# Performance work log

Measured on AMD Instinct MI355X. Metric: run time of the kernel, lower is better.

## Reference

```python
import jax, jax.numpy as jnp
import numpy as np

TAU = 1.0

def setup_inputs() -> dict:
    key = jax.random.key(0)
    k1, k2 = jax.random.split(key)
    b, t, n, e, top_k = 2, 64, 1024, 512, 256
    x = jax.random.normal(k1, (b, t, n, e), dtype=jnp.float32)
    # torch nn.Linear(embed_size, top_k): weight [top_k, e], bias [top_k]
    W = jax.random.normal(k2, (top_k, e), dtype=jnp.float32) * (1.0 / np.sqrt(e))
    b_bias = jnp.zeros((top_k,), dtype=jnp.float32)
    return {"x": x, "W": W, "b_bias": b_bias}

def reference(x, W, b_bias):
    b, t, n, e = x.shape
    x_flat = x.reshape(b, t * n, e)                 # [b, m, e], m = t*n
    scores = x_flat @ W.T + b_bias                  # [b, m, top_k]
    weights = jax.nn.softmax(scores / TAU, axis=1)  # softmax over token axis m
    # weighted-sum pooling for all top_k slots at once (replaces torch loop)
    selected = jnp.einsum('bmk,bme->bke', weights, x_flat)  # [b, top_k, e]
    return selected
```

## Files before the change

kernel.cpp:

```cpp
#include <hip/hip_runtime.h>
#include <stdint.h>

#define B_DIM 2
#define M_DIM 65536
#define E_DIM 512
#define K_DIM 256

typedef __bf16 bf16_t;
typedef __bf16 bf16x8 __attribute__((ext_vector_type(8)));
typedef float  f32x4  __attribute__((ext_vector_type(4)));

typedef const __attribute__((address_space(1))) void* gas_ptr;
typedef __attribute__((address_space(3))) void* las_ptr;

__device__ __forceinline__ void async_load16(const void* g, void* l) {
    __builtin_amdgcn_global_load_lds((gas_ptr)g, (las_ptr)l, 16, 0, 0);
}

__device__ __forceinline__ unsigned short bf16_bits(float f) {
    return __builtin_bit_cast(unsigned short, (__bf16)f);
}
__device__ __forceinline__ unsigned int pack2(float lo, float hi) {
    return (unsigned int)bf16_bits(lo) | ((unsigned int)bf16_bits(hi) << 16);
}

__global__ __launch_bounds__(256) void cast_w(const float* __restrict__ W, bf16_t* __restrict__ Wb) {
    int idx = blockIdx.x * 256 + threadIdx.x;
    float4 v = ((const float4*)W)[idx];
    ((uint2*)Wb)[idx] = make_uint2(pack2(v.x, v.y), pack2(v.z, v.w));
}

__global__ __launch_bounds__(256) void gemm1_exp_t(const float* __restrict__ x, const bf16_t* __restrict__ Wb,
                                                   bf16_t* __restrict__ pb, float* __restrict__ psums,
                                                   bf16_t* __restrict__ xT) {
    int gid = blockIdx.x;
    int mt = gid & 1023;
    int b  = gid >> 10;
    int m0 = mt * 64;
    int t = threadIdx.x, lane = t & 63, w = t >> 6;

    __shared__ __align__(16) char smem[40960];
    bf16_t* Alds = (bf16_t*)smem;
    bf16_t* Blds = (bf16_t*)(smem + 32768);
    bf16_t* Elds = (bf16_t*)smem;

    const float* xb = x + ((size_t)b * M_DIM + m0) * E_DIM;

    f32x4 zero = {0.f, 0.f, 0.f, 0.f};
    f32x4 acc[4][4];
#pragma unroll
    for (int i = 0; i < 4; ++i)
#pragma unroll
        for (int j = 0; j < 4; ++j) acc[i][j] = zero;

    int bst_r = t >> 2, bst_s0 = t & 3;

    int q = lane >> 4, r15 = lane & 15;

    for (int ke = 0; ke < 8; ++ke) {
        int e0 = ke * 64;
#pragma unroll
        for (int is = 0; is < 8; ++is) {
            int c = is * 256 + t;
            int row = c >> 3, sl = c & 7;
            int ge = sl ^ (row & 7);
            async_load16(Wb + (size_t)row * E_DIM + e0 + ge * 8, Alds + c * 8);
        }
#pragma unroll
        for (int sg = 0; sg < 2; ++sg) {
            int sl = bst_s0 + sg * 4;
            int ge = sl ^ (bst_r & 7);
            const float4* f = (const float4*)(xb + (size_t)bst_r * E_DIM + e0 + ge * 8);
            float4 a0 = f[0], a1 = f[1];
            *(uint4*)(Blds + bst_r * 64 + sl * 8) =
                make_uint4(pack2(a0.x, a0.y), pack2(a0.z, a0.w), pack2(a1.x, a1.y), pack2(a1.z, a1.w));
        }
        __syncthreads();

#pragma unroll
        for (int h = 0; h < 2; ++h) {
            bf16x8 af[4], bfr[4];
#pragma unroll
            for (int i = 0; i < 4; ++i) {
                int r = w * 64 + i * 16 + r15;
                int sl = (h * 4 + q) ^ (r & 7);
                af[i] = *(const bf16x8*)(Alds + r * 64 + sl * 8);
            }
#pragma unroll
            for (int j = 0; j < 4; ++j) {
                int r = j * 16 + r15;
                int sl = (h * 4 + q) ^ (r & 7);
                bfr[j] = *(const bf16x8*)(Blds + r * 64 + sl * 8);
            }
#pragma unroll
            for (int i = 0; i < 4; ++i)
#pragma unroll
                for (int j = 0; j < 4; ++j)
                    acc[i][j] = __builtin_amdgcn_mfma_f32_16x16x32_bf16(af[i], bfr[j], acc[i][j], 0, 0, 0);
        }

        {
            const unsigned short* Bs = (const unsigned short*)Blds;
            int l7 = t & 7;
            int mbase = l7 * 8;
            int ebase = t >> 3;
#pragma unroll
            for (int p = 0; p < 2; ++p) {
                int ecol = p * 32 + ebase;
                unsigned short vs[8];
#pragma unroll
                for (int s = 0; s < 8; ++s) {
                    int mmr = (s + l7) & 7;
                    int sl = (ecol >> 3) ^ mmr;
                    vs[mmr] = Bs[(mbase + mmr) * 64 + sl * 8 + (ecol & 7)];
                }
                uint4 u = make_uint4((unsigned)vs[0] | ((unsigned)vs[1] << 16),
                                     (unsigned)vs[2] | ((unsigned)vs[3] << 16),
                                     (unsigned)vs[4] | ((unsigned)vs[5] << 16),
                                     (unsigned)vs[6] | ((unsigned)vs[7] << 16));
                *(uint4*)(xT + ((size_t)(b * E_DIM + e0 + ecol)) * M_DIM + m0 + mbase) = u;
            }
        }
        __syncthreads();
    }

    int cc = lane & 15;
    float ksum[4][4];
#pragma unroll
    for (int i = 0; i < 4; ++i)
#pragma unroll
        for (int p = 0; p < 4; ++p) ksum[i][p] = 0.f;

#pragma unroll
    for (int i = 0; i < 4; ++i) {
        int kr = w * 64 + i * 16 + q * 4;
#pragma unroll
        for (int j = 0; j < 4; ++j) {
            int colb = j * 16 + cc;
            int g = colb >> 3, off = colb & 7;
#pragma unroll
            for (int p = 0; p < 4; ++p) {
                float v = __expf(acc[i][j][p]);
                ksum[i][p] += v;
                int k = kr + p;
                Elds[k * 64 + ((g ^ (k & 7)) * 8) + off] = (bf16_t)v;
            }
        }
    }
#pragma unroll
    for (int mask = 1; mask < 16; mask <<= 1)
#pragma unroll
        for (int i = 0; i < 4; ++i)
#pragma unroll
            for (int p = 0; p < 4; ++p)
                ksum[i][p] += __shfl_xor(ksum[i][p], mask, 64);
    if (cc == 0) {
        float* pp = psums + ((size_t)b * 1024 + mt) * 256;
#pragma unroll
        for (int i = 0; i < 4; ++i)
#pragma unroll
            for (int p = 0; p < 4; ++p)
                pp[w * 64 + i * 16 + q * 4 + p] = ksum[i][p];
    }
    __syncthreads();

    {
        int g = t & 7, rsub = t >> 3;
        uint4* dstb = (uint4*)(pb + (size_t)b * K_DIM * M_DIM + m0);
#pragma unroll
        for (int p = 0; p < 8; ++p) {
            int k = p * 32 + rsub;
            uint4 u = *(const uint4*)(Elds + k * 64 + ((g ^ (k & 7)) * 8));
            dstb[((size_t)k * M_DIM + g * 8) >> 3] = u;
        }
    }
}

__global__ __launch_bounds__(256) void gemm2(const bf16_t* __restrict__ pb, const bf16_t* __restrict__ xT,
                                             float* __restrict__ part) {
    int bid = blockIdx.x;
    int kt = bid & 1, et = (bid >> 1) & 3, ch = (bid >> 3) & 31, b = bid >> 8;
    int t = threadIdx.x, lane = t & 63, w = t >> 6;
    int wk = w & 1, we = w >> 1;

    __shared__ __align__(16) bf16_t Alds[128 * 64];
    __shared__ __align__(16) bf16_t Blds[128 * 64];

    const bf16_t* Ab = pb + ((size_t)(b * K_DIM + kt * 128)) * M_DIM + ch * 2048;
    const bf16_t* Bb = xT + ((size_t)(b * E_DIM + et * 128)) * M_DIM + ch * 2048;

    f32x4 zero = {0.f, 0.f, 0.f, 0.f};
    f32x4 acc[4][4];
#pragma unroll
    for (int i = 0; i < 4; ++i)
#pragma unroll
        for (int j = 0; j < 4; ++j) acc[i][j] = zero;

    int q = lane >> 4, r15 = lane & 15;

    for (int km = 0; km < 32; ++km) {
        int m0 = km * 64;
#pragma unroll
        for (int is = 0; is < 4; ++is) {
            int c = is * 256 + t;
            int row = c >> 3, sl = c & 7;
            int ge = sl ^ (row & 7);
            async_load16(Ab + (size_t)row * M_DIM + m0 + ge * 8, Alds + c * 8);
            async_load16(Bb + (size_t)row * M_DIM + m0 + ge * 8, Blds + c * 8);
        }
        __syncthreads();

#pragma unroll
        for (int h = 0; h < 2; ++h) {
            bf16x8 af[4], bfr[4];
#pragma unroll
            for (int i = 0; i < 4; ++i) {
                int r = wk * 64 + i * 16 + r15;
                int sl = (h * 4 + q) ^ (r & 7);
                af[i] = *(const bf16x8*)(Alds + r * 64 + sl * 8);
            }
#pragma unroll
            for (int j = 0; j < 4; ++j) {
                int r = we * 64 + j * 16 + r15;
                int sl = (h * 4 + q) ^ (r & 7);
                bfr[j] = *(const bf16x8*)(Blds + r * 64 + sl * 8);
            }
#pragma unroll
            for (int i = 0; i < 4; ++i)
#pragma unroll
                for (int j = 0; j < 4; ++j)
                    acc[i][j] = __builtin_amdgcn_mfma_f32_16x16x32_bf16(af[i], bfr[j], acc[i][j], 0, 0, 0);
        }
        __syncthreads();
    }

    float* pp = part + (size_t)bid * 16384;
    int cc = lane & 15;
#pragma unroll
    for (int i = 0; i < 4; ++i)
#pragma unroll
        for (int p = 0; p < 4; ++p) {
            int kl = wk * 64 + i * 16 + q * 4 + p;
#pragma unroll
            for (int j = 0; j < 4; ++j) {
                int el = we * 64 + j * 16 + cc;
                pp[kl * 128 + el] = acc[i][j][p];
            }
        }
}

__global__ __launch_bounds__(256) void reduce_out(const float* __restrict__ part, const float* __restrict__ psums,
                                                  float* __restrict__ out) {
    int bid = blockIdx.x;
    int ehalf = bid & 1, k = (bid >> 1) & 255, b = bid >> 9;
    int t = threadIdx.x, lane = t & 63;

    float cs = 0.f;
#pragma unroll
    for (int c = 0; c < 4; ++c) {
        int mt = c * 256 + t;
        cs += psums[((size_t)b * 1024 + mt) * 256 + k];
    }
#pragma unroll
    for (int mask = 1; mask < 64; mask <<= 1) cs += __shfl_xor(cs, mask, 64);
    __shared__ float cspart[4];
    if (lane == 0) cspart[t >> 6] = cs;
    __syncthreads();
    float colsum = (cspart[0] + cspart[1]) + (cspart[2] + cspart[3]);

    int e = ehalf * 256 + t;
    int kt = k >> 7, kl = k & 127, et = e >> 7, el = e & 127;
    float s = 0.f;
#pragma unroll
    for (int ch = 0; ch < 32; ++ch) {
        int bid2 = kt | (et << 1) | (ch << 3) | (b << 8);
        s += part[(size_t)bid2 * 16384 + kl * 128 + el];
    }
    out[((size_t)(b * 256 + k)) * 512 + e] = s / colsum;
}

extern "C" void kernel_launch(void* const* d_in, const int* in_sizes, int n_in,
                              void* d_out, int out_size, void* d_ws, size_t ws_size,
                              hipStream_t stream) {
    (void)in_sizes; (void)n_in; (void)out_size; (void)ws_size;
    const float* x = (const float*)d_in[0];
    const float* W = (const float*)d_in[1];

    char* ws = (char*)d_ws;
    bf16_t* xT    = (bf16_t*)ws;
    bf16_t* Wb    = (bf16_t*)(ws + 134217728);
    bf16_t* pb    = (bf16_t*)(ws + 134479872);
    float*  psums = (float*)(ws + 201588736);
    float*  part  = (float*)(ws + 203685888);
    float*  out   = (float*)d_out;

    cast_w<<<128, 256, 0, stream>>>(W, Wb);
    gemm1_exp_t<<<2048, 256, 0, stream>>>(x, Wb, pb, psums, xT);
    gemm2<<<512, 256, 0, stream>>>(pb, xT, part);
    reduce_out<<<1024, 256, 0, stream>>>(part, psums, out);
}
```

Measured before the change: 486.9 us.

## Store exp-weights and transposed x as FP8 and run second GEMM with FP8 MFMA

The intermediate exp-score matrix and the transposed copy of x are written as FP8 (e4m3/bf8 via cvt_pk_fp8) instead of bf16. The second GEMM then reads half the bytes and uses the fp8 MFMA instruction, with a new LDS swizzle for 8-byte fragments. This halves intermediate global traffic and increases MFMA throughput, but it sharply lowers precision of both operands, so accuracy may fall outside tolerance.

```diff
diff --git a/kernel.cpp b/kernel.cpp
--- a/kernel.cpp
+++ b/kernel.cpp
@@ -23,6 +23,16 @@
 __device__ __forceinline__ unsigned int pack2(float lo, float hi) {
     return (unsigned int)bf16_bits(lo) | ((unsigned int)bf16_bits(hi) << 16);
 }
+__device__ __forceinline__ float bf16u_to_f32(unsigned short us) {
+    return __builtin_bit_cast(float, (unsigned)us << 16);
+}
+__device__ __forceinline__ uint2 pack8_fp8(const float* f) {
+    int lo = __builtin_amdgcn_cvt_pk_fp8_f32(f[0], f[1], 0, false);
+    lo = __builtin_amdgcn_cvt_pk_fp8_f32(f[2], f[3], lo, true);
+    int hi = __builtin_amdgcn_cvt_pk_fp8_f32(f[4], f[5], 0, false);
+    hi = __builtin_amdgcn_cvt_pk_fp8_f32(f[6], f[7], hi, true);
+    return make_uint2((unsigned)lo, (unsigned)hi);
+}
 
 __global__ __launch_bounds__(256) void cast_w(const float* __restrict__ W, bf16_t* __restrict__ Wb) {
     int idx = blockIdx.x * 256 + threadIdx.x;
@@ -31,8 +41,8 @@
 }
 
 __global__ __launch_bounds__(256) void gemm1_exp_t(const float* __restrict__ x, const bf16_t* __restrict__ Wb,
-                                                   bf16_t* __restrict__ pb, float* __restrict__ psums,
-                                                   bf16_t* __restrict__ xT) {
+                                                   unsigned char* __restrict__ pb8, float* __restrict__ psums,
+                                                   unsigned char* __restrict__ xT8) {
     int gid = blockIdx.x;
     int mt = gid & 1023;
     int b  = gid >> 10;
@@ -107,18 +117,14 @@
 #pragma unroll
             for (int p = 0; p < 2; ++p) {
                 int ecol = p * 32 + ebase;
-                unsigned short vs[8];
+                float f[8];
 #pragma unroll
                 for (int s = 0; s < 8; ++s) {
                     int mmr = (s + l7) & 7;
                     int sl = (ecol >> 3) ^ mmr;
-                    vs[mmr] = Bs[(mbase + mmr) * 64 + sl * 8 + (ecol & 7)];
+                    f[mmr] = bf16u_to_f32(Bs[(mbase + mmr) * 64 + sl * 8 + (ecol & 7)]);
                 }
-                uint4 u = make_uint4((unsigned)vs[0] | ((unsigned)vs[1] << 16),
-                                     (unsigned)vs[2] | ((unsigned)vs[3] << 16),
-                                     (unsigned)vs[4] | ((unsigned)vs[5] << 16),
-                                     (unsigned)vs[6] | ((unsigned)vs[7] << 16));
-                *(uint4*)(xT + ((size_t)(b * E_DIM + e0 + ecol)) * M_DIM + m0 + mbase) = u;
+                *(uint2*)(xT8 + ((size_t)(b * E_DIM + e0 + ecol)) * M_DIM + m0 + mbase) = pack8_fp8(f);
             }
         }
         __syncthreads();
@@ -166,28 +172,31 @@
 
     {
         int g = t & 7, rsub = t >> 3;
-        uint4* dstb = (uint4*)(pb + (size_t)b * K_DIM * M_DIM + m0);
+        unsigned char* dstb = pb8 + (size_t)b * K_DIM * M_DIM + m0;
 #pragma unroll
         for (int p = 0; p < 8; ++p) {
             int k = p * 32 + rsub;
-            uint4 u = *(const uint4*)(Elds + k * 64 + ((g ^ (k & 7)) * 8));
-            dstb[((size_t)k * M_DIM + g * 8) >> 3] = u;
-        }
-    }
-}
-
-__global__ __launch_bounds__(256) void gemm2(const bf16_t* __restrict__ pb, const bf16_t* __restrict__ xT,
+            const unsigned short* src = (const unsigned short*)(Elds + k * 64 + ((g ^ (k & 7)) * 8));
+            float f[8];
+#pragma unroll
+            for (int s = 0; s < 8; ++s) f[s] = bf16u_to_f32(src[s]);
+            *(uint2*)(dstb + (size_t)k * M_DIM + g * 8) = pack8_fp8(f);
+        }
+    }
+}
+
+__global__ __launch_bounds__(256) void gemm2(const unsigned char* __restrict__ pb8, const unsigned char* __restrict__ xT8,
                                              float* __restrict__ part) {
     int bid = blockIdx.x;
     int kt = bid & 1, et = (bid >> 1) & 3, ch = (bid >> 3) & 31, b = bid >> 8;
     int t = threadIdx.x, lane = t & 63, w = t >> 6;
     int wk = w & 1, we = w >> 1;
 
-    __shared__ __align__(16) bf16_t Alds[128 * 64];
-    __shared__ __align__(16) bf16_t Blds[128 * 64];
-
-    const bf16_t* Ab = pb + ((size_t)(b * K_DIM + kt * 128)) * M_DIM + ch * 2048;
-    const bf16_t* Bb = xT + ((size_t)(b * E_DIM + et * 128)) * M_DIM + ch * 2048;
+    __shared__ __align__(16) unsigned char Alds[128 * 64];
+    __shared__ __align__(16) unsigned char Blds[128 * 64];
+
+    const unsigned char* Ab = pb8 + ((size_t)(b * K_DIM + kt * 128)) * M_DIM + ch * 2048;
+    const unsigned char* Bb = xT8 + ((size_t)(b * E_DIM + et * 128)) * M_DIM + ch * 2048;
 
     f32x4 zero = {0.f, 0.f, 0.f, 0.f};
     f32x4 acc[4][4];
@@ -201,35 +210,40 @@
     for (int km = 0; km < 32; ++km) {
         int m0 = km * 64;
 #pragma unroll
-        for (int is = 0; is < 4; ++is) {
+        for (int is = 0; is < 2; ++is) {
             int c = is * 256 + t;
-            int row = c >> 3, sl = c & 7;
-            int ge = sl ^ (row & 7);
-            async_load16(Ab + (size_t)row * M_DIM + m0 + ge * 8, Alds + c * 8);
-            async_load16(Bb + (size_t)row * M_DIM + m0 + ge * 8, Blds + c * 8);
+            int row = c >> 2, a = c & 3;
+            int sr = (row & 3) ^ ((row >> 2) & 3);
+            int bsl = a ^ sr;
+            async_load16(Ab + (size_t)row * M_DIM + m0 + bsl * 16, Alds + c * 16);
+            async_load16(Bb + (size_t)row * M_DIM + m0 + bsl * 16, Blds + c * 16);
         }
         __syncthreads();
 
 #pragma unroll
         for (int h = 0; h < 2; ++h) {
-            bf16x8 af[4], bfr[4];
+            long av[4], bv[4];
 #pragma unroll
             for (int i = 0; i < 4; ++i) {
-                int r = wk * 64 + i * 16 + r15;
-                int sl = (h * 4 + q) ^ (r & 7);
-                af[i] = *(const bf16x8*)(Alds + r * 64 + sl * 8);
+                int r = wk * 128 / 2 * 0 + wk * 64 + i * 16 + r15;
+                int sr = (r & 3) ^ ((r >> 2) & 3);
+                int g = h * 4 + q;
+                int off = (((g >> 1) ^ sr) * 16) + (g & 1) * 8;
+                av[i] = *(const long*)(Alds + r * 64 + off);
             }
 #pragma unroll
             for (int j = 0; j < 4; ++j) {
                 int r = we * 64 + j * 16 + r15;
-                int sl = (h * 4 + q) ^ (r & 7);
-                bfr[j] = *(const bf16x8*)(Blds + r * 64 + sl * 8);
+                int sr = (r & 3) ^ ((r >> 2) & 3);
+                int g = h * 4 + q;
+                int off = (((g >> 1) ^ sr) * 16) + (g & 1) * 8;
+                bv[j] = *(const long*)(Blds + r * 64 + off);
             }
 #pragma unroll
             for (int i = 0; i < 4; ++i)
 #pragma unroll
                 for (int j = 0; j < 4; ++j)
-                    acc[i][j] = __builtin_amdgcn_mfma_f32_16x16x32_bf16(af[i], bfr[j], acc[i][j], 0, 0, 0);
+                    acc[i][j] = __builtin_amdgcn_mfma_f32_16x16x32_fp8_fp8(av[i], bv[j], acc[i][j], 0, 0, 0);
         }
         __syncthreads();
     }
@@ -287,15 +301,15 @@
     const float* W = (const float*)d_in[1];
 
     char* ws = (char*)d_ws;
-    bf16_t* xT    = (bf16_t*)ws;
-    bf16_t* Wb    = (bf16_t*)(ws + 134217728);
-    bf16_t* pb    = (bf16_t*)(ws + 134479872);
-    float*  psums = (float*)(ws + 201588736);
-    float*  part  = (float*)(ws + 203685888);
+    unsigned char* xT8 = (unsigned char*)ws;
+    bf16_t* Wb    = (bf16_t*)(ws + 67108864);
+    unsigned char* pb8 = (unsigned char*)(ws + 67371008);
+    float*  psums = (float*)(ws + 100925440);
+    float*  part  = (float*)(ws + 103022592);
     float*  out   = (float*)d_out;
 
     cast_w<<<128, 256, 0, stream>>>(W, Wb);
-    gemm1_exp_t<<<2048, 256, 0, stream>>>(x, Wb, pb, psums, xT);
-    gemm2<<<512, 256, 0, stream>>>(pb, xT, part);
+    gemm1_exp_t<<<2048, 256, 0, stream>>>(x, Wb, pb8, psums, xT8);
+    gemm2<<<512, 256, 0, stream>>>(pb8, xT8, part);
     reduce_out<<<1024, 256, 0, stream>>>(part, psums, out);
 }
```

Result: faster. 441.2 us (-9.4%).
